# Kernel optimization log

Measured on AMD Instinct MI355X. Metric: run time of the kernel, lower is better.

## Reference

```python
import jax, jax.numpy as jnp
import numpy as np

E = 4          # num_experts
B = 32         # batch
CIN = 64
COUT = 64
H = 112
WID = 112
K = 3          # kernel size


def setup_inputs() -> dict:
    key = jax.random.key(0)
    k1, k2, k3, k4 = jax.random.split(key, 4)
    x = jax.random.normal(k1, (B, CIN, H, WID), dtype=jnp.float32)
    layer_mask = jax.random.uniform(k2, (B, E), dtype=jnp.float32)
    # per-expert conv weights/biases (kaiming-ish scale)
    W = jax.random.normal(k3, (E, COUT, CIN, K, K), dtype=jnp.float32) * 0.05
    b = jax.random.normal(k4, (E, COUT), dtype=jnp.float32) * 0.05
    return {"x": x, "layer_mask": layer_mask, "W": W, "b": b}


def _conv(x, w):
    # stride 1, padding 1 on both spatial dims (matches nn.Conv2d(k=3, s=1, p=1))
    return jax.lax.conv_general_dilated(
        x, w, window_strides=(1, 1), padding=[(1, 1), (1, 1)],
        dimension_numbers=("NCHW", "OIHW", "NCHW"))


def reference(x, layer_mask, W, b):
    # Loop over the small fixed expert set, accumulating the gated sum to
    # avoid materializing an [E, B, C, H, W] intermediate.
    out = jnp.zeros((B, COUT, H, WID), dtype=x.dtype)
    for e in range(E):
        expert_out = _conv(x, W[e]) + b[e][None, :, None, None]
        gate = layer_mask[:, e][:, None, None, None]  # [B,1,1,1]
        out = out + expert_out * gate
    return out
```

## Files before the change

kernel.cpp:

```cpp
#include <hip/hip_runtime.h>
#include <stdint.h>

#define CIN   64
#define COUT  64
#define HH    112
#define WW    112
#define NEXP  4
#define HW    (HH * WW)

typedef short bf16x8 __attribute__((ext_vector_type(8)));
typedef float f32x16 __attribute__((ext_vector_type(16)));

__device__ inline uint16_t f2bf(float f) {
    uint32_t u = __builtin_bit_cast(uint32_t, f);
    return (uint16_t)((u + 0x7FFFu + ((u >> 16) & 1u)) >> 16);
}

__global__ __launch_bounds__(256)
void fold_wb(const float* __restrict__ W, const float* __restrict__ bias,
             const float* __restrict__ mask,
             uint16_t* __restrict__ Weff, float* __restrict__ Beff, int B) {
    int idx = blockIdx.x * 256 + threadIdx.x;
    if (idx >= B * 72 * 512) return;
    int j   = idx & 7;
    int co  = (idx >> 3) & 63;
    int g   = (idx >> 9) % 72;
    int n   = idx / (512 * 72);
    int par   = g & 1;
    int kq    = (g >> 1) & 1;
    int khw   = (g >> 2) % 9;
    int phase = (g >> 2) / 9;
    int ci = phase * 32 + (kq * 2 + par) * 8 + j;
    float acc = 0.f;
#pragma unroll
    for (int e = 0; e < NEXP; ++e)
        acc = fmaf(mask[n * NEXP + e],
                   W[((size_t)(e * COUT + co) * CIN + ci) * 9 + khw], acc);
    Weff[idx] = f2bf(acc);
    if (g == 0 && j == 0) {
        float ba = 0.f;
#pragma unroll
        for (int e = 0; e < NEXP; ++e)
            ba = fmaf(mask[n * NEXP + e], bias[e * COUT + co], ba);
        Beff[n * COUT + co] = ba;
    }
}

__device__ inline void stage_phase(const float* __restrict__ xph,
                                   uint16_t* __restrict__ buf,
                                   int h0, int w0, int tid) {
    for (int u = tid; u < 3456; u += 256) {
        int p     = u % 6;
        int rowid = u / 6;
        int dh  = rowid % 18;
        int cio = rowid / 18;
        int h = h0 + dh - 1;
        int wbase = w0 - 4 + p * 4;
        bool hok = (unsigned)h < (unsigned)HH;
        bool lok = hok && (wbase >= 0) && (wbase <= WW - 4);
        float4 v = {0.f, 0.f, 0.f, 0.f};
        if (lok)
            v = *(const float4*)(xph + (size_t)cio * HW + h * WW + wbase);
        float vv[4] = {v.x, v.y, v.z, v.w};
        const int o = cio >> 3, cl = cio & 7;
#pragma unroll
        for (int m = 0; m < 4; ++m) {
            int dw = p * 4 + m - 3;
            if ((unsigned)dw < 18u) {
                int w = w0 - 1 + dw;
                float val = (hok && (unsigned)w < (unsigned)WW) ? vv[m] : 0.f;
                int pix = dh * 18 + dw;
                int s = o ^ ((pix >> 1) & 3);
                buf[pix * 32 + s * 8 + cl] = f2bf(val);
            }
        }
    }
}

__device__ inline void compute_phase(const uint16_t* __restrict__ buf,
                                     const uint16_t* __restrict__ wp,
                                     int rowb, int colb, int par,
                                     f32x16& acc00, f32x16& acc01,
                                     f32x16& acc10, f32x16& acc11) {
#pragma unroll 3
    for (int khw = 0; khw < 9; ++khw) {
        const int dh = khw / 3;
        const int dw = khw - dh * 3;
        const int pb0 = (rowb + dh) * 18 + (colb + dw);
        const int pb1 = pb0 + 36;
        const int f0 = (pb0 >> 1) & 3, f1 = (pb1 >> 1) & 3;
        const uint16_t* lp0 = &buf[pb0 * 32];
        const uint16_t* lp1 = &buf[pb1 * 32];
#pragma unroll
        for (int kq = 0; kq < 2; ++kq) {
            const int cgA = kq * 2 + par;
            bf16x8 b0 = *(const bf16x8*)(lp0 + ((cgA ^ f0) << 3));
            bf16x8 b1 = *(const bf16x8*)(lp1 + ((cgA ^ f1) << 3));
            const uint16_t* wk = wp + (size_t)((khw * 2 + kq) * 2) * 512;
            bf16x8 a0 = *(const bf16x8*)(wk);
            bf16x8 a1 = *(const bf16x8*)(wk + 256);
            acc00 = __builtin_amdgcn_mfma_f32_32x32x16_bf16(a0, b0, acc00, 0, 0, 0);
            acc01 = __builtin_amdgcn_mfma_f32_32x32x16_bf16(a0, b1, acc01, 0, 0, 0);
            acc10 = __builtin_amdgcn_mfma_f32_32x32x16_bf16(a1, b0, acc10, 0, 0, 0);
            acc11 = __builtin_amdgcn_mfma_f32_32x32x16_bf16(a1, b1, acc11, 0, 0, 0);
        }
    }
}

__global__ __launch_bounds__(256, 3)
void conv_fused(const float* __restrict__ x, const uint16_t* __restrict__ Weff,
                const float* __restrict__ Beff, float* __restrict__ out,
                int nwg) {
    __shared__ uint16_t ldsx[324 * 32];

    int bid = blockIdx.x;
    if ((nwg & 7) == 0)
        bid = (bid & 7) * (nwg >> 3) + (bid >> 3);

    const int tid  = threadIdx.x;
    const int lane = tid & 63;
    const int wid  = tid >> 6;
    const int tileIdx = bid % 49;
    const int n  = bid / 49;
    const int th = tileIdx / 7, tw = tileIdx % 7;
    const int h0 = th * 16, w0 = tw * 16;

    const int rowb = wid * 4 + ((lane & 31) >> 4);
    const int colb = lane & 15;
    const int par  = lane >> 5;

    const uint16_t* wbase = Weff + (size_t)n * 36864
                          + (size_t)par * 512 + (size_t)(lane & 31) * 8;
    const float* xn = x + (size_t)n * CIN * HW;

    f32x16 acc00 = {}, acc01 = {}, acc10 = {}, acc11 = {};

#pragma unroll
    for (int phase = 0; phase < 2; ++phase) {
        if (phase) __syncthreads();
        stage_phase(xn + (size_t)phase * 32 * HW, ldsx, h0, w0, tid);
        __syncthreads();
        compute_phase(ldsx, wbase + (size_t)phase * 36 * 512,
                      rowb, colb, par, acc00, acc01, acc10, acc11);
    }

    const float* bptr = Beff + n * 64;
    const int row0 = h0 + rowb;
    const int col  = w0 + colb;
#pragma unroll
    for (int r = 0; r < 16; ++r) {
        const int co = (r & 3) + 8 * (r >> 2) + 4 * par;
        const float bia0 = bptr[co];
        const float bia1 = bptr[co + 32];
        size_t o00 = ((size_t)(n * COUT + co) * HH + row0) * WW + col;
        __builtin_nontemporal_store(acc00[r] + bia0, &out[o00]);
        __builtin_nontemporal_store(acc01[r] + bia0, &out[o00 + 2 * WW]);
        size_t o10 = o00 + (size_t)32 * HW;
        __builtin_nontemporal_store(acc10[r] + bia1, &out[o10]);
        __builtin_nontemporal_store(acc11[r] + bia1, &out[o10 + 2 * WW]);
    }
}

#define COB   8
#define PIX_PER_BLK 256
#define NTILE (HW / PIX_PER_BLK)

__global__ void fold_weights(const float* __restrict__ W,
                             const float* __restrict__ mask,
                             float* __restrict__ Weff, int B) {
    int idx = blockIdx.x * blockDim.x + threadIdx.x;
    int total = B * CIN * 9 * COUT;
    if (idx >= total) return;
    int co = idx % COUT;
    int t  = idx / COUT;
    int k  = t % 9;
    t /= 9;
    int ci = t % CIN;
    int n  = t / CIN;
    float acc = 0.f;
#pragma unroll
    for (int e = 0; e < NEXP; ++e)
        acc = fmaf(mask[n * NEXP + e],
                   W[(((size_t)(e * COUT + co) * CIN + ci) * 9) + k], acc);
    Weff[idx] = acc;
}

__global__ __launch_bounds__(PIX_PER_BLK, 4)
void conv_gated(const float* __restrict__ x,
                const float* __restrict__ mask,
                const float* __restrict__ bias,
                const float* __restrict__ Weff,
                float* __restrict__ out) {
    const int tile = blockIdx.x % NTILE;
    const int cob  = (blockIdx.x / NTILE) % (COUT / COB);
    const int n    = blockIdx.x / (NTILE * (COUT / COB));
    const int p = tile * PIX_PER_BLK + threadIdx.x;
    const int h = p / WW;
    const int w = p % WW;
    const int co0 = cob * COB;

    float acc[COB];
#pragma unroll
    for (int j = 0; j < COB; ++j) {
        float a = 0.f;
#pragma unroll
        for (int e = 0; e < NEXP; ++e)
            a = fmaf(mask[n * NEXP + e], bias[e * COUT + co0 + j], a);
        acc[j] = a;
    }

    const float* xb = x + (((size_t)n * CIN) * HH + h) * WW + w;
    const float* wb = Weff + ((size_t)n * CIN) * 9 * COUT + co0;
    const bool rok0 = (h > 0), rok2 = (h < HH - 1);
    const bool cok0 = (w > 0), cok2 = (w < WW - 1);

    for (int ci = 0; ci < CIN; ++ci) {
        const float* xc = xb + (size_t)ci * HW;
        const float* wc = wb + (size_t)ci * 9 * COUT;
#pragma unroll
        for (int kh = 0; kh < 3; ++kh) {
            const bool rok = (kh == 0) ? rok0 : ((kh == 2) ? rok2 : true);
#pragma unroll
            for (int kw = 0; kw < 3; ++kw) {
                const bool cok = (kw == 0) ? cok0 : ((kw == 2) ? cok2 : true);
                float xv = (rok && cok) ? xc[(kh - 1) * WW + (kw - 1)] : 0.f;
                const float4* wk = (const float4*)(wc + (kh * 3 + kw) * COUT);
                float4 wa = wk[0], wb4 = wk[1];
                acc[0] = fmaf(xv, wa.x, acc[0]);
                acc[1] = fmaf(xv, wa.y, acc[1]);
                acc[2] = fmaf(xv, wa.z, acc[2]);
                acc[3] = fmaf(xv, wa.w, acc[3]);
                acc[4] = fmaf(xv, wb4.x, acc[4]);
                acc[5] = fmaf(xv, wb4.y, acc[5]);
                acc[6] = fmaf(xv, wb4.z, acc[6]);
                acc[7] = fmaf(xv, wb4.w, acc[7]);
            }
        }
    }
    float* ob = out + (((size_t)(n * COUT + co0)) * HH + h) * WW + w;
#pragma unroll
    for (int j = 0; j < COB; ++j)
        ob[(size_t)j * HW] = acc[j];
}

extern "C" void kernel_launch(void* const* d_in, const int* in_sizes, int n_in,
                              void* d_out, int out_size, void* d_ws, size_t ws_size,
                              hipStream_t stream) {
    const float* x    = (const float*)d_in[0];
    const float* mask = (const float*)d_in[1];
    const float* W    = (const float*)d_in[2];
    const float* b    = (const float*)d_in[3];
    float* out = (float*)d_out;

    const int B = in_sizes[0] / (CIN * HW);
    const size_t weffB = (size_t)B * 36864 * 2;
    const size_t beffB = (size_t)B * COUT * 4;
    const size_t need  = weffB + beffB;

    if (ws_size >= need) {
        uint16_t* Weff = (uint16_t*)d_ws;
        float*    Beff = (float*)((char*)d_ws + weffB);
        int foldBlocks = (B * 72 * 512 + 255) / 256;
        fold_wb<<<foldBlocks, 256, 0, stream>>>(W, b, mask, Weff, Beff, B);
        const int nwg = B * 49;
        conv_fused<<<nwg, 256, 0, stream>>>(x, Weff, Beff, out, nwg);
    } else {
        float* Weff = (float*)d_ws;
        const size_t weff_elems = (size_t)B * CIN * 9 * COUT;
        int foldBlocks = (int)((weff_elems + 255) / 256);
        fold_weights<<<foldBlocks, 256, 0, stream>>>(W, mask, Weff, B);
        conv_gated<<<B * (COUT / COB) * NTILE, PIX_PER_BLK, 0, stream>>>(
            x, mask, b, Weff, out);
    }
}
```

Before: 82.77 us.

## Pre-transform input to padded NHWC bf16 and stage tiles via global_load_lds

Adds a separate pass that converts x into a zero-padded NHWC bf16 buffer in workspace. The conv kernel then loads its whole 18x18x64 halo tile at once with direct global-to-LDS loads, replacing the per-phase fp32 gather, conversion and extra barrier. This aims to cut staging overhead and issue pressure in the conv kernel, at the cost of an extra kernel launch and a full read plus bf16 write of the input through global memory. It also doubles LDS per block, which may reduce occupancy.

```diff
diff --git a/kernel.cpp b/kernel.cpp
--- a/kernel.cpp
+++ b/kernel.cpp
@@ -14,6 +14,45 @@
 __device__ inline uint16_t f2bf(float f) {
     uint32_t u = __builtin_bit_cast(uint32_t, f);
     return (uint16_t)((u + 0x7FFFu + ((u >> 16) & 1u)) >> 16);
+}
+
+__device__ __forceinline__ void gll16(const uint16_t* g, uint16_t* l) {
+    __builtin_amdgcn_global_load_lds(
+        (const __attribute__((address_space(1))) uint32_t*)g,
+        (__attribute__((address_space(3))) uint32_t*)l, 16, 0, 0);
+}
+
+__global__ __launch_bounds__(256)
+void xform_x(const float* __restrict__ x, uint16_t* __restrict__ Xt) {
+    __shared__ float lds[CIN][WW + 1];
+    const int hp = blockIdx.x % 114;
+    const int n  = blockIdx.x / 114;
+    const int h  = hp - 1;
+    uint16_t* orow = Xt + ((size_t)(n * 114 + hp)) * 114 * 64;
+
+    if (h < 0 || h >= HH) {
+        const uint4 z = {0, 0, 0, 0};
+        for (int u = threadIdx.x; u < 114 * 8; u += 256)
+            *(uint4*)(orow + u * 8) = z;
+        return;
+    }
+    for (int i = threadIdx.x; i < CIN * WW; i += 256) {
+        int ci = i / WW, w = i % WW;
+        lds[ci][w] = x[((size_t)(n * CIN + ci)) * HW + h * WW + w];
+    }
+    __syncthreads();
+    for (int u = threadIdx.x; u < 114 * 8; u += 256) {
+        int wp = u >> 3, cg = u & 7;
+        int w = wp - 1;
+        union { uint16_t s[8]; uint4 v; } pk;
+        if (w < 0 || w >= WW) {
+            pk.v = (uint4){0, 0, 0, 0};
+        } else {
+#pragma unroll
+            for (int j = 0; j < 8; ++j) pk.s[j] = f2bf(lds[cg * 8 + j][w]);
+        }
+        *(uint4*)(orow + (size_t)u * 8) = pk.v;
+    }
 }
 
 __global__ __launch_bounds__(256)
@@ -46,37 +85,6 @@
     }
 }
 
-__device__ inline void stage_phase(const float* __restrict__ xph,
-                                   uint16_t* __restrict__ buf,
-                                   int h0, int w0, int tid) {
-    for (int u = tid; u < 3456; u += 256) {
-        int p     = u % 6;
-        int rowid = u / 6;
-        int dh  = rowid % 18;
-        int cio = rowid / 18;
-        int h = h0 + dh - 1;
-        int wbase = w0 - 4 + p * 4;
-        bool hok = (unsigned)h < (unsigned)HH;
-        bool lok = hok && (wbase >= 0) && (wbase <= WW - 4);
-        float4 v = {0.f, 0.f, 0.f, 0.f};
-        if (lok)
-            v = *(const float4*)(xph + (size_t)cio * HW + h * WW + wbase);
-        float vv[4] = {v.x, v.y, v.z, v.w};
-        const int o = cio >> 3, cl = cio & 7;
-#pragma unroll
-        for (int m = 0; m < 4; ++m) {
-            int dw = p * 4 + m - 3;
-            if ((unsigned)dw < 18u) {
-                int w = w0 - 1 + dw;
-                float val = (hok && (unsigned)w < (unsigned)WW) ? vv[m] : 0.f;
-                int pix = dh * 18 + dw;
-                int s = o ^ ((pix >> 1) & 3);
-                buf[pix * 32 + s * 8 + cl] = f2bf(val);
-            }
-        }
-    }
-}
-
 __device__ inline void compute_phase(const uint16_t* __restrict__ buf,
                                      const uint16_t* __restrict__ wp,
                                      int rowb, int colb, int par,
@@ -108,10 +116,10 @@
 }
 
 __global__ __launch_bounds__(256, 3)
-void conv_fused(const float* __restrict__ x, const uint16_t* __restrict__ Weff,
-                const float* __restrict__ Beff, float* __restrict__ out,
-                int nwg) {
-    __shared__ uint16_t ldsx[324 * 32];
+void conv_gll(const uint16_t* __restrict__ Xt, const uint16_t* __restrict__ Weff,
+              const float* __restrict__ Beff, float* __restrict__ out,
+              int nwg) {
+    __shared__ uint16_t ldsx[2592 * 8];
 
     int bid = blockIdx.x;
     if ((nwg & 7) == 0)
@@ -125,24 +133,44 @@
     const int th = tileIdx / 7, tw = tileIdx % 7;
     const int h0 = th * 16, w0 = tw * 16;
 
+    const uint16_t* xt_n = Xt + (size_t)n * (114 * 114 * 64);
+
+#pragma unroll
+    for (int it = 0; it < 10; ++it) {
+        int u  = it * 256 + tid;
+        int ph = (u >= 1296) ? 1 : 0;
+        int v  = u - ph * 1296;
+        int pix = v >> 2, s = v & 3;
+        int dh = pix / 18, dw = pix - dh * 18;
+        int cg = s ^ ((pix >> 1) & 3);
+        const uint16_t* src = xt_n + ((size_t)(h0 + dh) * 114 + (w0 + dw)) * 64
+                            + ph * 32 + cg * 8;
+        uint16_t* dst = ldsx + (size_t)(it * 256 + wid * 64) * 8;
+        gll16(src, dst);
+    }
+    if (tid < 32) {
+        int v = 1264 + tid;
+        int pix = v >> 2, s = v & 3;
+        int dh = pix / 18, dw = pix - dh * 18;
+        int cg = s ^ ((pix >> 1) & 3);
+        const uint16_t* src = xt_n + ((size_t)(h0 + dh) * 114 + (w0 + dw)) * 64
+                            + 32 + cg * 8;
+        *(uint4*)(ldsx + (size_t)(2560 + tid) * 8) = *(const uint4*)src;
+    }
+    __syncthreads();
+
     const int rowb = wid * 4 + ((lane & 31) >> 4);
     const int colb = lane & 15;
     const int par  = lane >> 5;
 
     const uint16_t* wbase = Weff + (size_t)n * 36864
                           + (size_t)par * 512 + (size_t)(lane & 31) * 8;
-    const float* xn = x + (size_t)n * CIN * HW;
 
     f32x16 acc00 = {}, acc01 = {}, acc10 = {}, acc11 = {};
-
-#pragma unroll
-    for (int phase = 0; phase < 2; ++phase) {
-        if (phase) __syncthreads();
-        stage_phase(xn + (size_t)phase * 32 * HW, ldsx, h0, w0, tid);
-        __syncthreads();
-        compute_phase(ldsx, wbase + (size_t)phase * 36 * 512,
-                      rowb, colb, par, acc00, acc01, acc10, acc11);
-    }
+    compute_phase(ldsx,         wbase,                rowb, colb, par,
+                  acc00, acc01, acc10, acc11);
+    compute_phase(ldsx + 10368, wbase + 36 * 512,     rowb, colb, par,
+                  acc00, acc01, acc10, acc11);
 
     const float* bptr = Beff + n * 64;
     const int row0 = h0 + rowb;
@@ -255,15 +283,18 @@
     const int B = in_sizes[0] / (CIN * HW);
     const size_t weffB = (size_t)B * 36864 * 2;
     const size_t beffB = (size_t)B * COUT * 4;
-    const size_t need  = weffB + beffB;
+    const size_t xtB   = (size_t)B * 114 * 114 * 64 * 2;
+    const size_t need  = weffB + beffB + xtB;
 
     if (ws_size >= need) {
         uint16_t* Weff = (uint16_t*)d_ws;
         float*    Beff = (float*)((char*)d_ws + weffB);
+        uint16_t* Xt   = (uint16_t*)((char*)d_ws + weffB + beffB);
         int foldBlocks = (B * 72 * 512 + 255) / 256;
         fold_wb<<<foldBlocks, 256, 0, stream>>>(W, b, mask, Weff, Beff, B);
+        xform_x<<<B * 114, 256, 0, stream>>>(x, Xt);
         const int nwg = B * 49;
-        conv_fused<<<nwg, 256, 0, stream>>>(x, Weff, Beff, out, nwg);
+        conv_gll<<<nwg, 256, 0, stream>>>(Xt, Weff, Beff, out, nwg);
     } else {
         float* Weff = (float*)d_ws;
         const size_t weff_elems = (size_t)B * CIN * 9 * COUT;
```

Result: slower. 93.13 us (+12.5%).
